# Kernel optimization log

Measured on AMD Instinct MI355X. Metric: run time of the kernel, lower is better.

Reference implementation:

```python
import jax, jax.numpy as jnp
import numpy as np

DIM = 1024
HEADS = 16
DIM_HEAD = 64
INNER = HEADS * DIM_HEAD
LN_EPS = 1e-5


def setup_inputs() -> dict:
    key = jax.random.key(0)
    ks = jax.random.split(key, 7)
    b, n = 2, 2048
    x = jax.random.normal(ks[0], (b, n, DIM), dtype=jnp.float32)
    attn_bias = jax.random.normal(ks[1], (HEADS, n, n), dtype=jnp.float32)
    gamma = jnp.ones((DIM,), dtype=jnp.float32)
    beta = jnp.zeros((DIM,), dtype=jnp.float32)
    wq = jax.random.normal(ks[2], (DIM, INNER), dtype=jnp.float32) * (DIM ** -0.5)
    wkv = jax.random.normal(ks[3], (DIM, 2 * INNER), dtype=jnp.float32) * (DIM ** -0.5)
    wo = jax.random.normal(ks[4], (INNER, DIM), dtype=jnp.float32) * (INNER ** -0.5)
    return {"x": x, "attn_bias": attn_bias, "gamma": gamma, "beta": beta,
            "wq": wq, "wkv": wkv, "wo": wo}


def reference(x, attn_bias, gamma, beta, wq, wkv, wo):
    b, n, _ = x.shape
    scale = DIM_HEAD ** -0.5
    # LayerNorm
    mu = jnp.mean(x, axis=-1, keepdims=True)
    var = jnp.var(x, axis=-1, keepdims=True)
    xn = (x - mu) * jax.lax.rsqrt(var + LN_EPS) * gamma + beta
    # QKV projections
    q = xn @ wq                      # [b, n, inner]
    kv = xn @ wkv                    # [b, n, 2*inner]
    k, v = jnp.split(kv, 2, axis=-1)
    split_heads = lambda t: t.reshape(b, n, HEADS, DIM_HEAD).transpose(0, 2, 1, 3)
    q, k, v = map(split_heads, (q, k, v))  # [b, h, n, d]
    q = q * scale
    sim = jnp.einsum('bhid,bhjd->bhij', q, k)
    sim = sim + attn_bias[None]      # broadcast over batch
    causal_mask = jnp.triu(jnp.ones((n, n), dtype=bool), k=1)
    sim = jnp.where(causal_mask, -jnp.finfo(sim.dtype).max, sim)
    attn = jax.nn.softmax(sim, axis=-1)
    out = jnp.einsum('bhij,bhjd->bhid', attn, v)
    out = out.transpose(0, 2, 1, 3).reshape(b, n, INNER)
    return out @ wo
```

## Files before the change

### kernel.cpp

```cpp
#include <hip/hip_runtime.h>
#include <hip/hip_bf16.h>

#define DIM   1024
#define HEADS 16
#define DHEAD 64
#define INNER 1024
#define NSEQ  2048
#define NB    2
#define MROWS (NB * NSEQ)
#define QS    (3 * INNER)

typedef __attribute__((ext_vector_type(8))) short    short8;
typedef __attribute__((ext_vector_type(4))) short    short4v;
typedef __attribute__((ext_vector_type(4))) float    floatx4;
typedef __attribute__((ext_vector_type(8))) _Float16 half8;

#define GLOBAL_AS __attribute__((address_space(1)))
#define LDS_AS    __attribute__((address_space(3)))

static __device__ __forceinline__ short f2h(float f) {
  _Float16 h = (_Float16)f;
  return __builtin_bit_cast(short, h);
}
static __device__ __forceinline__ float h2f(short s) {
  return (float)__builtin_bit_cast(_Float16, s);
}

static __device__ __forceinline__ floatx4 mfma16(short8 a, short8 b, floatx4 c) {
  return __builtin_amdgcn_mfma_f32_16x16x32_f16(
      __builtin_bit_cast(half8, a), __builtin_bit_cast(half8, b), c, 0, 0, 0);
}

__global__ __launch_bounds__(256) void ln_kernel(const float* __restrict__ x,
                                                 const float* __restrict__ gamma,
                                                 const float* __restrict__ beta,
                                                 short* __restrict__ xn) {
  int row = blockIdx.x;
  int t   = threadIdx.x;
  const float4* xr = reinterpret_cast<const float4*>(x + (size_t)row * DIM);
  float4 v = xr[t];
  float s  = v.x + v.y + v.z + v.w;
  float s2 = v.x * v.x + v.y * v.y + v.z * v.z + v.w * v.w;
#pragma unroll
  for (int off = 1; off < 64; off <<= 1) {
    s  += __shfl_xor(s, off);
    s2 += __shfl_xor(s2, off);
  }
  __shared__ float red[8];
  if ((t & 63) == 0) { red[t >> 6] = s; red[(t >> 6) + 4] = s2; }
  __syncthreads();
  s  = red[0] + red[1] + red[2] + red[3];
  s2 = red[4] + red[5] + red[6] + red[7];
  float mu   = s * (1.0f / DIM);
  float var  = s2 * (1.0f / DIM) - mu * mu;
  float rstd = rsqrtf(var + 1e-5f);
  float4 g  = reinterpret_cast<const float4*>(gamma)[t];
  float4 bb = reinterpret_cast<const float4*>(beta)[t];
  short4v o;
  o.x = f2h((v.x - mu) * rstd * g.x + bb.x);
  o.y = f2h((v.y - mu) * rstd * g.y + bb.y);
  o.z = f2h((v.z - mu) * rstd * g.z + bb.z);
  o.w = f2h((v.w - mu) * rstd * g.w + bb.w);
  reinterpret_cast<short4v*>(xn + (size_t)row * DIM)[t] = o;
}

__global__ __launch_bounds__(256) void transpose_f16(const float* __restrict__ w,
                                                     short* __restrict__ wt,
                                                     int Kk, int Nn) {
  __shared__ float tile[32][33];
  int n0 = blockIdx.x * 32, k0 = blockIdx.y * 32;
  int tx = threadIdx.x & 31, ty = threadIdx.x >> 5;
#pragma unroll
  for (int i = 0; i < 32; i += 8)
    tile[ty + i][tx] = w[(size_t)(k0 + ty + i) * Nn + n0 + tx];
  __syncthreads();
#pragma unroll
  for (int i = 0; i < 32; i += 8)
    wt[(size_t)(n0 + ty + i) * Kk + k0 + tx] = f2h(tile[tx][ty + i]);
}

template <bool F32OUT>
__global__ __launch_bounds__(256) void gemm_bt(const short* __restrict__ A,
                                               const short* __restrict__ Bt,
                                               void* __restrict__ Cout,
                                               int Nn, int Kk,
                                               float oscale, float oscale2,
                                               int qsplit) {
  constexpr int BM = 128, BN = 128, BK = 64;
  __shared__ __attribute__((aligned(16))) short As[BM * BK];
  __shared__ __attribute__((aligned(16))) short Bs[BN * BK];
  int bm = blockIdx.x, bn = blockIdx.y;
  int t = threadIdx.x, lane = t & 63, w = t >> 6;
  int l15 = lane & 15, lhi = lane >> 4;
  int wr = w >> 1, wc = w & 1;
  float osc = (bn * BN < qsplit) ? oscale : oscale2;
  floatx4 acc[4][4] = {};
  const short* Ag = A + (size_t)bm * BM * Kk;
  const short* Bg = Bt + (size_t)bn * BN * Kk;

  for (int k0 = 0; k0 < Kk; k0 += BK) {
#pragma unroll
    for (int it = 0; it < 4; ++it) {
      int base = it * 256 + w * 64;
      int idx  = base + lane;
      int row  = idx >> 3, kc = (idx & 7) << 3;
      __builtin_amdgcn_global_load_lds(
          (const GLOBAL_AS unsigned int*)(Ag + (size_t)row * Kk + k0 + kc),
          (LDS_AS unsigned int*)(As + base * 8), 16, 0, 0);
    }
#pragma unroll
    for (int it = 0; it < 4; ++it) {
      int base = it * 256 + w * 64;
      int idx  = base + lane;
      int row  = idx >> 3, kc = (idx & 7) << 3;
      __builtin_amdgcn_global_load_lds(
          (const GLOBAL_AS unsigned int*)(Bg + (size_t)row * Kk + k0 + kc),
          (LDS_AS unsigned int*)(Bs + base * 8), 16, 0, 0);
    }
    __syncthreads();
#pragma unroll
    for (int kc = 0; kc < 2; ++kc) {
      short8 a[4], b[4];
#pragma unroll
      for (int mt = 0; mt < 4; ++mt)
        a[mt] = *reinterpret_cast<const short8*>(
            &As[(wr * 64 + mt * 16 + l15) * BK + lhi * 8 + kc * 32]);
#pragma unroll
      for (int nt = 0; nt < 4; ++nt)
        b[nt] = *reinterpret_cast<const short8*>(
            &Bs[(wc * 64 + nt * 16 + l15) * BK + lhi * 8 + kc * 32]);
#pragma unroll
      for (int mt = 0; mt < 4; ++mt)
#pragma unroll
        for (int nt = 0; nt < 4; ++nt)
          acc[mt][nt] = mfma16(a[mt], b[nt], acc[mt][nt]);
    }
    __syncthreads();
  }

  int row0 = bm * BM + wr * 64;
  int col0 = bn * BN + wc * 64;
#pragma unroll
  for (int mt = 0; mt < 4; ++mt)
#pragma unroll
    for (int nt = 0; nt < 4; ++nt)
#pragma unroll
      for (int r = 0; r < 4; ++r) {
        int row = row0 + mt * 16 + lhi * 4 + r;
        int col = col0 + nt * 16 + l15;
        if (F32OUT)
          ((float*)Cout)[(size_t)row * Nn + col] = acc[mt][nt][r] * osc;
        else
          ((short*)Cout)[(size_t)row * Nn + col] = f2h(acc[mt][nt][r] * osc);
      }
}

__global__ __launch_bounds__(256) void attn_kernel(const short* __restrict__ qkv,
                                                   const float* __restrict__ bias,
                                                   short* __restrict__ Opart,
                                                   float* __restrict__ mlpart) {
  constexpr int LDK = 72;
  __shared__ __attribute__((aligned(16))) short Ks[2][64 * LDK];
  __shared__ __attribute__((aligned(16))) short Vt[2][64 * LDK];
  __shared__ __attribute__((aligned(16))) short Ps[64 * LDK];
  int id = blockIdx.x, h = blockIdx.y, b = blockIdx.z;
  int qt, c;
  if (id < 32)      { c = 0; qt = 31 - id; }
  else if (id < 56) { c = 1; qt = 63 - id; }
  else if (id < 72) { c = 2; qt = 87 - id; }
  else              { c = 3; qt = 103 - id; }
  int tt0 = c * 8;
  int tt1 = (tt0 + 8 < qt + 1) ? (tt0 + 8) : (qt + 1);
  int qb = qt * 64;
  int t = threadIdx.x, lane = t & 63, w = t >> 6;
  int l15 = lane & 15, lhi = lane >> 4;

  const short* qrow =
      qkv + ((size_t)(b * NSEQ + qb + w * 16 + l15)) * QS + h * DHEAD + lhi * 8;
  short8 qf0 = *reinterpret_cast<const short8*>(qrow);
  short8 qf1 = *reinterpret_cast<const short8*>(qrow + 32);

  int krow = t >> 3, kcol = (t & 7) << 3;
  int rr = (t >> 3) * 2, cc = (t & 7) << 3;
  short8 kr0, kr1, vr0, vr1;

  auto issue_kv = [&](int tile) {
    int j0 = tile * 64;
    const short* kp =
        qkv + ((size_t)(b * NSEQ + j0 + krow)) * QS + INNER + h * DHEAD + kcol;
    kr0 = *reinterpret_cast<const short8*>(kp);
    kr1 = *reinterpret_cast<const short8*>(kp + (size_t)32 * QS);
    const short* vp = qkv + ((size_t)(b * NSEQ + j0 + rr)) * QS +
                      2 * INNER + h * DHEAD + cc;
    vr0 = *reinterpret_cast<const short8*>(vp);
    vr1 = *reinterpret_cast<const short8*>(vp + QS);
  };
  auto issue_bias = [&](int tile, floatx4 (&br)[4]) {
    const float* bb =
        bias + ((size_t)h * NSEQ + (qb + w * 16 + l15)) * NSEQ + tile * 64 + lhi * 4;
#pragma unroll
    for (int jt = 0; jt < 4; ++jt)
      br[jt] = *reinterpret_cast<const floatx4*>(bb + jt * 16);
  };
  auto writeKV = [&](int buf) {
    *reinterpret_cast<short8*>(&Ks[buf][krow * LDK + kcol]) = kr0;
    *reinterpret_cast<short8*>(&Ks[buf][(krow + 32) * LDK + kcol]) = kr1;
#pragma unroll
    for (int e = 0; e < 8; ++e) {
      int d  = cc + e;
      int jj = rr ^ (((d >> 3) & 7) << 3);
      unsigned int pk = (unsigned short)vr0[e] |
                        ((unsigned int)(unsigned short)vr1[e] << 16);
      *reinterpret_cast<unsigned int*>(&Vt[buf][d * LDK + jj]) = pk;
    }
  };

  float m = -1e30f, l = 0.f;
  floatx4 oacc[4] = {};

  auto step = [&](int tt, int buf, floatx4 (&br)[4]) {
    if (tt + 1 < tt1) issue_kv(tt + 1);
    __syncthreads();

    floatx4 s[4];
#pragma unroll
    for (int jt = 0; jt < 4; ++jt) s[jt] = br[jt];
    if (tt + 2 < tt1) issue_bias(tt + 2, br);

#pragma unroll
    for (int jt = 0; jt < 4; ++jt) {
      short8 kf0 = *reinterpret_cast<const short8*>(
          &Ks[buf][(jt * 16 + l15) * LDK + lhi * 8]);
      short8 kf1 = *reinterpret_cast<const short8*>(
          &Ks[buf][(jt * 16 + l15) * LDK + lhi * 8 + 32]);
      s[jt] = mfma16(kf0, qf0, s[jt]);
      s[jt] = mfma16(kf1, qf1, s[jt]);
    }

    if (tt == qt) {
#pragma unroll
      for (int jt = 0; jt < 4; ++jt)
#pragma unroll
        for (int r = 0; r < 4; ++r) {
          int jloc = jt * 16 + lhi * 4 + r;
          if (jloc > w * 16 + l15) s[jt][r] = -1e30f;
        }
    }

    float mx = s[0][0];
#pragma unroll
    for (int jt = 0; jt < 4; ++jt)
#pragma unroll
      for (int r = 0; r < 4; ++r) mx = fmaxf(mx, s[jt][r]);
    mx = fmaxf(mx, __shfl_xor(mx, 16));
    mx = fmaxf(mx, __shfl_xor(mx, 32));
    float mnew = fmaxf(m, mx);
    float fac  = __expf(m - mnew);
    m = mnew;
    float ps = 0.f;
#pragma unroll
    for (int jt = 0; jt < 4; ++jt)
#pragma unroll
      for (int r = 0; r < 4; ++r) {
        float pv = __expf(s[jt][r] - mnew);
        s[jt][r] = pv;
        ps += pv;
      }
    ps += __shfl_xor(ps, 16);
    ps += __shfl_xor(ps, 32);
    l = l * fac + ps;

    float facr[4];
#pragma unroll
    for (int r = 0; r < 4; ++r)
      facr[r] = __shfl(fac, (lane & 48) | (lhi * 4 + r));
#pragma unroll
    for (int dt = 0; dt < 4; ++dt)
#pragma unroll
      for (int r = 0; r < 4; ++r) oacc[dt][r] *= facr[r];

#pragma unroll
    for (int jt = 0; jt < 4; ++jt) {
      short4v pv4;
      pv4.x = f2h(s[jt][0]); pv4.y = f2h(s[jt][1]);
      pv4.z = f2h(s[jt][2]); pv4.w = f2h(s[jt][3]);
      *reinterpret_cast<short4v*>(
          &Ps[(w * 16 + l15) * LDK + jt * 16 + lhi * 4]) = pv4;
    }

#pragma unroll
    for (int jc = 0; jc < 2; ++jc) {
      short8 pf = *reinterpret_cast<const short8*>(
          &Ps[(w * 16 + l15) * LDK + lhi * 8 + jc * 32]);
#pragma unroll
      for (int dt = 0; dt < 4; ++dt) {
        int dd = dt * 16 + l15;
        int jj = (lhi * 8 + jc * 32) ^ (((dd >> 3) & 7) << 3);
        short8 vf = *reinterpret_cast<const short8*>(&Vt[buf][dd * LDK + jj]);
        oacc[dt] = mfma16(pf, vf, oacc[dt]);
      }
    }

    if (tt + 1 < tt1) writeKV(buf ^ 1);
  };

  floatx4 brA[4], brB[4];
  issue_kv(tt0);
  issue_bias(tt0, brA);
  if (tt0 + 1 < tt1) issue_bias(tt0 + 1, brB);
  writeKV(0);

  int nt = tt1 - tt0;
  for (int i = 0; i < nt; i += 2) {
    step(tt0 + i, 0, brA);
    if (i + 1 < nt) step(tt0 + i + 1, 1, brB);
  }

  size_t p = (size_t)(b * HEADS + h) * 80 + id;
  short* Ob = Opart + p * 4096;
#pragma unroll
  for (int dt = 0; dt < 4; ++dt)
#pragma unroll
    for (int r = 0; r < 4; ++r)
      Ob[(w * 16 + lhi * 4 + r) * 64 + dt * 16 + l15] = f2h(oacc[dt][r]);
  if (lhi == 0) {
    mlpart[p * 128 + w * 16 + l15] = m;
    mlpart[p * 128 + 64 + w * 16 + l15] = l;
  }
}

__global__ __launch_bounds__(256) void attn_combine(const short* __restrict__ Opart,
                                                    const float* __restrict__ mlpart,
                                                    short* __restrict__ o) {
  int qt = blockIdx.x, h = blockIdx.y, b = blockIdx.z;
  int nc = qt / 8 + 1;
  int t = threadIdx.x, row = t >> 2, cg = (t & 3) << 4;
  size_t base = (size_t)(b * HEADS + h) * 80;
  const int idtab[4] = {31, 63, 87, 103};

  float M = -1e30f;
  float mv0 = 0, mv1 = 0, mv2 = 0, mv3 = 0, lv0 = 0, lv1 = 0, lv2 = 0, lv3 = 0;
  {
    size_t p = base + idtab[0] - qt;
    mv0 = mlpart[p * 128 + row]; lv0 = mlpart[p * 128 + 64 + row];
    M = mv0;
  }
  if (nc > 1) { size_t p = base + idtab[1] - qt;
    mv1 = mlpart[p * 128 + row]; lv1 = mlpart[p * 128 + 64 + row]; M = fmaxf(M, mv1); }
  if (nc > 2) { size_t p = base + idtab[2] - qt;
    mv2 = mlpart[p * 128 + row]; lv2 = mlpart[p * 128 + 64 + row]; M = fmaxf(M, mv2); }
  if (nc > 3) { size_t p = base + idtab[3] - qt;
    mv3 = mlpart[p * 128 + row]; lv3 = mlpart[p * 128 + 64 + row]; M = fmaxf(M, mv3); }

  float acc[16] = {};
  float lsum = 0.f;
#pragma unroll
  for (int c2 = 0; c2 < 4; ++c2) {
    if (c2 >= nc) break;
    float mc = (c2 == 0) ? mv0 : (c2 == 1) ? mv1 : (c2 == 2) ? mv2 : mv3;
    float lc = (c2 == 0) ? lv0 : (c2 == 1) ? lv1 : (c2 == 2) ? lv2 : lv3;
    float wgt = __expf(mc - M);
    lsum += wgt * lc;
    size_t p = base + idtab[c2] - qt;
    const short8* Or =
        reinterpret_cast<const short8*>(Opart + p * 4096 + row * 64 + cg);
    short8 a0 = Or[0], a1 = Or[1];
#pragma unroll
    for (int e = 0; e < 8; ++e) {
      acc[e]     += wgt * h2f(a0[e]);
      acc[8 + e] += wgt * h2f(a1[e]);
    }
  }
  float inv = 1.f / lsum;
  short* op = o + ((size_t)(b * NSEQ + qt * 64 + row)) * INNER + h * DHEAD + cg;
  short8 o0, o1;
#pragma unroll
  for (int e = 0; e < 8; ++e) {
    o0[e] = f2h(acc[e] * inv);
    o1[e] = f2h(acc[8 + e] * inv);
  }
  reinterpret_cast<short8*>(op)[0] = o0;
  reinterpret_cast<short8*>(op)[1] = o1;
}

extern "C" void kernel_launch(void* const* d_in, const int* in_sizes, int n_in,
                              void* d_out, int out_size, void* d_ws, size_t ws_size,
                              hipStream_t stream) {
  const float* x     = (const float*)d_in[0];
  const float* bias  = (const float*)d_in[1];
  const float* gamma = (const float*)d_in[2];
  const float* beta  = (const float*)d_in[3];
  const float* wq    = (const float*)d_in[4];
  const float* wkv   = (const float*)d_in[5];
  const float* wo    = (const float*)d_in[6];
  float* out = (float*)d_out;

  char* ws = (char*)d_ws;
  const size_t MB = 1024 * 1024;
  short* xn      = (short*)(ws);
  short* wqkv_t  = (short*)(ws + 8  * MB);
  short* wo_t    = (short*)(ws + 14 * MB);
  short* qkv     = (short*)(ws + 16 * MB);
  short* Opart   = (short*)(ws + 40 * MB);
  float* mlpart  = (float*)(ws + 60 * MB);
  short* ao      = xn;

  ln_kernel<<<MROWS, 256, 0, stream>>>(x, gamma, beta, xn);
  transpose_f16<<<dim3(INNER / 32, DIM / 32), 256, 0, stream>>>(wq, wqkv_t, DIM, INNER);
  transpose_f16<<<dim3(2 * INNER / 32, DIM / 32), 256, 0, stream>>>(
      wkv, wqkv_t + (size_t)1024 * 1024, DIM, 2 * INNER);
  transpose_f16<<<dim3(DIM / 32, INNER / 32), 256, 0, stream>>>(wo, wo_t, INNER, DIM);

  gemm_bt<false><<<dim3(MROWS / 128, QS / 128), 256, 0, stream>>>(
      xn, wqkv_t, qkv, QS, DIM, 0.125f, 1.0f, 1024);

  attn_kernel<<<dim3(80, HEADS, NB), 256, 0, stream>>>(qkv, bias, Opart, mlpart);
  attn_combine<<<dim3(32, HEADS, NB), 256, 0, stream>>>(Opart, mlpart, ao);

  gemm_bt<true><<<dim3(MROWS / 128, DIM / 128), 256, 0, stream>>>(
      ao, wo_t, out, DIM, INNER, 1.0f, 1.0f, 0);
}
```

Before: 175.0 us.

## Double attention query tile to 128 rows with 512-thread blocks and table-driven scheduling

The attention kernel now handles 128 query rows per block with 8 waves. Each K/V tile loaded into LDS is therefore shared by twice as many queries, roughly halving K/V global and LDS traffic per query. Work is split into 40 (qtile, chunk) items per head, scheduled through constant lookup tables that order blocks so the heaviest items go first and batches interleave. The combine kernel is adjusted for the new partial layout. The cost is higher register and LDS use per block and coarser load balance across the causal triangle.

```diff
diff --git a/kernel.cpp b/kernel.cpp
--- a/kernel.cpp
+++ b/kernel.cpp
@@ -30,6 +30,28 @@
   return __builtin_amdgcn_mfma_f32_16x16x32_f16(
       __builtin_bit_cast(half8, a), __builtin_bit_cast(half8, b), c, 0, 0, 0);
 }
+
+__device__ __constant__ signed char kQtTab[40] = {
+  15,14,13,12,11,10,9,8,7,6,5,4,3,
+  15,14,13,12,11,10,9,8,7,
+  15,14,13,12,11,
+  15,
+  2,6,10,14,
+  1,5,9,13,
+  0,4,8,12};
+__device__ __constant__ signed char kCTab[40] = {
+  0,0,0,0,0,0,0,0,0,0,0,0,0,
+  1,1,1,1,1,1,1,1,1,
+  2,2,2,2,2,
+  3,
+  0,1,2,3,
+  0,1,2,3,
+  0,1,2,3};
+__device__ __constant__ signed char kSlotTab[16][4] = {
+  {36,-1,-1,-1},{32,-1,-1,-1},{28,-1,-1,-1},{12,-1,-1,-1},
+  {11,37,-1,-1},{10,33,-1,-1},{ 9,29,-1,-1},{ 8,21,-1,-1},
+  { 7,20,38,-1},{ 6,19,34,-1},{ 5,18,30,-1},{ 4,17,26,-1},
+  { 3,16,25,39},{ 2,15,24,35},{ 1,14,23,31},{ 0,13,22,27}};
 
 __global__ __launch_bounds__(256) void ln_kernel(const float* __restrict__ x,
                                                  const float* __restrict__ gamma,
@@ -155,23 +177,25 @@
       }
 }
 
-__global__ __launch_bounds__(256) void attn_kernel(const short* __restrict__ qkv,
+__global__ __launch_bounds__(512) void attn_kernel(const short* __restrict__ qkv,
                                                    const float* __restrict__ bias,
                                                    short* __restrict__ Opart,
                                                    float* __restrict__ mlpart) {
   constexpr int LDK = 72;
   __shared__ __attribute__((aligned(16))) short Ks[2][64 * LDK];
   __shared__ __attribute__((aligned(16))) short Vt[2][64 * LDK];
-  __shared__ __attribute__((aligned(16))) short Ps[64 * LDK];
-  int id = blockIdx.x, h = blockIdx.y, b = blockIdx.z;
-  int qt, c;
-  if (id < 32)      { c = 0; qt = 31 - id; }
-  else if (id < 56) { c = 1; qt = 63 - id; }
-  else if (id < 72) { c = 2; qt = 87 - id; }
-  else              { c = 3; qt = 103 - id; }
+  __shared__ __attribute__((aligned(16))) short Ps[128 * LDK];
+
+  int g = blockIdx.x;
+  int gg = g >> 4, slot = g & 15;
+  int b = slot >> 3;
+  int p = gg * 8 + (slot & 7);
+  int h = p / 40, id = p % 40;
+  int qt = kQtTab[id], c = kCTab[id];
   int tt0 = c * 8;
-  int tt1 = (tt0 + 8 < qt + 1) ? (tt0 + 8) : (qt + 1);
-  int qb = qt * 64;
+  int tt1 = 2 * qt + 2; if (tt0 + 8 < tt1) tt1 = tt0 + 8;
+  int qb = qt * 128;
+
   int t = threadIdx.x, lane = t & 63, w = t >> 6;
   int l15 = lane & 15, lhi = lane >> 4;
 
@@ -181,19 +205,18 @@
   short8 qf1 = *reinterpret_cast<const short8*>(qrow + 32);
 
   int krow = t >> 3, kcol = (t & 7) << 3;
-  int rr = (t >> 3) * 2, cc = (t & 7) << 3;
-  short8 kr0, kr1, vr0, vr1;
+  int vrr = (t >> 4) * 2, vcc = (t & 15) << 2;
+  short8 kr;
+  short4v vr0, vr1;
 
   auto issue_kv = [&](int tile) {
     int j0 = tile * 64;
-    const short* kp =
-        qkv + ((size_t)(b * NSEQ + j0 + krow)) * QS + INNER + h * DHEAD + kcol;
-    kr0 = *reinterpret_cast<const short8*>(kp);
-    kr1 = *reinterpret_cast<const short8*>(kp + (size_t)32 * QS);
-    const short* vp = qkv + ((size_t)(b * NSEQ + j0 + rr)) * QS +
-                      2 * INNER + h * DHEAD + cc;
-    vr0 = *reinterpret_cast<const short8*>(vp);
-    vr1 = *reinterpret_cast<const short8*>(vp + QS);
+    kr = *reinterpret_cast<const short8*>(
+        qkv + ((size_t)(b * NSEQ + j0 + krow)) * QS + INNER + h * DHEAD + kcol);
+    const short* vp = qkv + ((size_t)(b * NSEQ + j0 + vrr)) * QS +
+                      2 * INNER + h * DHEAD + vcc;
+    vr0 = *reinterpret_cast<const short4v*>(vp);
+    vr1 = *reinterpret_cast<const short4v*>(vp + QS);
   };
   auto issue_bias = [&](int tile, floatx4 (&br)[4]) {
     const float* bb =
@@ -203,12 +226,11 @@
       br[jt] = *reinterpret_cast<const floatx4*>(bb + jt * 16);
   };
   auto writeKV = [&](int buf) {
-    *reinterpret_cast<short8*>(&Ks[buf][krow * LDK + kcol]) = kr0;
-    *reinterpret_cast<short8*>(&Ks[buf][(krow + 32) * LDK + kcol]) = kr1;
-#pragma unroll
-    for (int e = 0; e < 8; ++e) {
-      int d  = cc + e;
-      int jj = rr ^ (((d >> 3) & 7) << 3);
+    *reinterpret_cast<short8*>(&Ks[buf][krow * LDK + kcol]) = kr;
+#pragma unroll
+    for (int e = 0; e < 4; ++e) {
+      int d  = vcc + e;
+      int jj = vrr ^ (((d >> 3) & 7) << 3);
       unsigned int pk = (unsigned short)vr0[e] |
                         ((unsigned int)(unsigned short)vr1[e] << 16);
       *reinterpret_cast<unsigned int*>(&Vt[buf][d * LDK + jj]) = pk;
@@ -237,13 +259,14 @@
       s[jt] = mfma16(kf1, qf1, s[jt]);
     }
 
-    if (tt == qt) {
+    if (tt >= 2 * qt) {
+      int dq = qb + w * 16 + l15 - tt * 64;
 #pragma unroll
       for (int jt = 0; jt < 4; ++jt)
 #pragma unroll
         for (int r = 0; r < 4; ++r) {
           int jloc = jt * 16 + lhi * 4 + r;
-          if (jloc > w * 16 + l15) s[jt][r] = -1e30f;
+          if (jloc > dq) s[jt][r] = -1e30f;
         }
     }
 
@@ -307,63 +330,58 @@
   floatx4 brA[4], brB[4];
   issue_kv(tt0);
   issue_bias(tt0, brA);
-  if (tt0 + 1 < tt1) issue_bias(tt0 + 1, brB);
+  issue_bias(tt0 + 1, brB);
   writeKV(0);
 
   int nt = tt1 - tt0;
   for (int i = 0; i < nt; i += 2) {
     step(tt0 + i, 0, brA);
-    if (i + 1 < nt) step(tt0 + i + 1, 1, brB);
-  }
-
-  size_t p = (size_t)(b * HEADS + h) * 80 + id;
-  short* Ob = Opart + p * 4096;
+    step(tt0 + i + 1, 1, brB);
+  }
+
+  size_t pp = (size_t)(b * HEADS + h) * 40 + id;
+  short* Ob = Opart + pp * 8192;
 #pragma unroll
   for (int dt = 0; dt < 4; ++dt)
 #pragma unroll
     for (int r = 0; r < 4; ++r)
       Ob[(w * 16 + lhi * 4 + r) * 64 + dt * 16 + l15] = f2h(oacc[dt][r]);
   if (lhi == 0) {
-    mlpart[p * 128 + w * 16 + l15] = m;
-    mlpart[p * 128 + 64 + w * 16 + l15] = l;
-  }
-}
-
-__global__ __launch_bounds__(256) void attn_combine(const short* __restrict__ Opart,
+    mlpart[pp * 256 + w * 16 + l15] = m;
+    mlpart[pp * 256 + 128 + w * 16 + l15] = l;
+  }
+}
+
+__global__ __launch_bounds__(512) void attn_combine(const short* __restrict__ Opart,
                                                     const float* __restrict__ mlpart,
                                                     short* __restrict__ o) {
   int qt = blockIdx.x, h = blockIdx.y, b = blockIdx.z;
-  int nc = qt / 8 + 1;
+  int nc = qt / 4 + 1;
   int t = threadIdx.x, row = t >> 2, cg = (t & 3) << 4;
-  size_t base = (size_t)(b * HEADS + h) * 80;
-  const int idtab[4] = {31, 63, 87, 103};
-
+  size_t base = (size_t)(b * HEADS + h) * 40;
+
+  float mv[4], lv[4];
   float M = -1e30f;
-  float mv0 = 0, mv1 = 0, mv2 = 0, mv3 = 0, lv0 = 0, lv1 = 0, lv2 = 0, lv3 = 0;
-  {
-    size_t p = base + idtab[0] - qt;
-    mv0 = mlpart[p * 128 + row]; lv0 = mlpart[p * 128 + 64 + row];
-    M = mv0;
-  }
-  if (nc > 1) { size_t p = base + idtab[1] - qt;
-    mv1 = mlpart[p * 128 + row]; lv1 = mlpart[p * 128 + 64 + row]; M = fmaxf(M, mv1); }
-  if (nc > 2) { size_t p = base + idtab[2] - qt;
-    mv2 = mlpart[p * 128 + row]; lv2 = mlpart[p * 128 + 64 + row]; M = fmaxf(M, mv2); }
-  if (nc > 3) { size_t p = base + idtab[3] - qt;
-    mv3 = mlpart[p * 128 + row]; lv3 = mlpart[p * 128 + 64 + row]; M = fmaxf(M, mv3); }
+#pragma unroll
+  for (int c2 = 0; c2 < 4; ++c2) {
+    if (c2 < nc) {
+      size_t p = base + kSlotTab[qt][c2];
+      mv[c2] = mlpart[p * 256 + row];
+      lv[c2] = mlpart[p * 256 + 128 + row];
+      M = fmaxf(M, mv[c2]);
+    }
+  }
 
   float acc[16] = {};
   float lsum = 0.f;
 #pragma unroll
   for (int c2 = 0; c2 < 4; ++c2) {
     if (c2 >= nc) break;
-    float mc = (c2 == 0) ? mv0 : (c2 == 1) ? mv1 : (c2 == 2) ? mv2 : mv3;
-    float lc = (c2 == 0) ? lv0 : (c2 == 1) ? lv1 : (c2 == 2) ? lv2 : lv3;
-    float wgt = __expf(mc - M);
-    lsum += wgt * lc;
-    size_t p = base + idtab[c2] - qt;
+    float wgt = __expf(mv[c2] - M);
+    lsum += wgt * lv[c2];
+    size_t p = base + kSlotTab[qt][c2];
     const short8* Or =
-        reinterpret_cast<const short8*>(Opart + p * 4096 + row * 64 + cg);
+        reinterpret_cast<const short8*>(Opart + p * 8192 + row * 64 + cg);
     short8 a0 = Or[0], a1 = Or[1];
 #pragma unroll
     for (int e = 0; e < 8; ++e) {
@@ -372,7 +390,7 @@
     }
   }
   float inv = 1.f / lsum;
-  short* op = o + ((size_t)(b * NSEQ + qt * 64 + row)) * INNER + h * DHEAD + cg;
+  short* op = o + ((size_t)(b * NSEQ + qt * 128 + row)) * INNER + h * DHEAD + cg;
   short8 o0, o1;
 #pragma unroll
   for (int e = 0; e < 8; ++e) {
@@ -402,7 +420,7 @@
   short* wo_t    = (short*)(ws + 14 * MB);
   short* qkv     = (short*)(ws + 16 * MB);
   short* Opart   = (short*)(ws + 40 * MB);
-  float* mlpart  = (float*)(ws + 60 * MB);
+  float* mlpart  = (float*)(ws + 62 * MB);
   short* ao      = xn;
 
   ln_kernel<<<MROWS, 256, 0, stream>>>(x, gamma, beta, xn);
@@ -414,8 +432,8 @@
   gemm_bt<false><<<dim3(MROWS / 128, QS / 128), 256, 0, stream>>>(
       xn, wqkv_t, qkv, QS, DIM, 0.125f, 1.0f, 1024);
 
-  attn_kernel<<<dim3(80, HEADS, NB), 256, 0, stream>>>(qkv, bias, Opart, mlpart);
-  attn_combine<<<dim3(32, HEADS, NB), 256, 0, stream>>>(Opart, mlpart, ao);
+  attn_kernel<<<1280, 512, 0, stream>>>(qkv, bias, Opart, mlpart);
+  attn_combine<<<dim3(16, HEADS, NB), 512, 0, stream>>>(Opart, mlpart, ao);
 
   gemm_bt<true><<<dim3(MROWS / 128, DIM / 128), 256, 0, stream>>>(
       ao, wo_t, out, DIM, INNER, 1.0f, 1.0f, 0);
```

After: 180.3 us. 1.03x slower.
